# Performance work log

Measured on AMD Instinct MI355X. Metric: run time of the kernel, lower is better.

Reference implementation:

```python
import jax, jax.numpy as jnp
import numpy as np

B, O, GRID = 2048, 48, 112
SIGMA = 5.0


def setup_inputs() -> dict:
    key = jax.random.key(0)
    k1, k2, k3, k4, k5 = jax.random.split(key, 5)
    s = float(GRID - 1)
    xL = jax.random.uniform(k1, (B,), dtype=jnp.float32) * s
    yL = jax.random.uniform(k2, (B,), dtype=jnp.float32) * s
    obj_list = jax.random.uniform(k3, (B, O, 2), dtype=jnp.float32) * s
    obj_num = jax.random.randint(k4, (B,), 0, O + 1, dtype=jnp.int32)
    road_mask = jax.random.randint(k5, (B, GRID, GRID), 0, 2, dtype=jnp.int32)
    return {"xL": xL, "yL": yL, "obj_list": obj_list, "obj_num": obj_num,
            "road_mask": road_mask, "H": GRID, "W": GRID}


def reference(xL, yL, obj_list, obj_num, road_mask, H, W):
    # Faithful vectorization of batch_gaussian_tensor_obj.
    # exp(-(dx^2+dy^2)/(2s^2)) is separable: exp(-dx^2/..) * exp(-dy^2/..),
    # so per-object splats reduce to a batched matmul over the object axis.
    inv = 1.0 / (2.0 * SIGMA * SIGMA)
    x = jnp.arange(H, dtype=jnp.float32)  # row coordinate grid
    y = jnp.arange(W, dtype=jnp.float32)  # col coordinate grid

    # positive goal gaussian, rank-1 outer product per batch element
    gx = jnp.exp(-((x[None, :] - xL[:, None]) ** 2) * inv)  # [B,H]
    gy = jnp.exp(-((y[None, :] - yL[:, None]) ** 2) * inv)  # [B,W]
    goal = gx[:, :, None] * gy[:, None, :]                   # [B,H,W]

    # negative object gaussians; note original swaps xy: xo=xy[1], yo=xy[0]
    xo = obj_list[:, :, 1]  # [B,O] row coords
    yo = obj_list[:, :, 0]  # [B,O] col coords
    ex = jnp.exp(-((x[None, None, :] - xo[:, :, None]) ** 2) * inv)  # [B,O,H]
    ey = jnp.exp(-((y[None, None, :] - yo[:, :, None]) ** 2) * inv)  # [B,O,W]
    valid = (jnp.arange(O)[None, :] < obj_num[:, None]).astype(jnp.float32)  # [B,O]
    obj = jnp.einsum('boh,bow->bhw', ex * valid[:, :, None], ey)     # [B,H,W]

    channel = 0.5 + 0.5 * goal - 0.5 * obj
    channel = jnp.where(road_mask == 0, 0.0, channel)
    return channel
```

## Files before the change

### kernel.cpp

```cpp
#include <hip/hip_runtime.h>

#define GRID_N 112
#define O_MAX 48
#define HW_N (GRID_N * GRID_N)
#define NT 512
#define KPAD 64
#define LSTR 72

typedef _Float16 half8  __attribute__((ext_vector_type(8)));
typedef _Float16 half2v __attribute__((ext_vector_type(2)));
typedef float    f32x4  __attribute__((ext_vector_type(4)));

__global__ __launch_bounds__(NT) void goalmap_kernel(
    const float* __restrict__ xL, const float* __restrict__ yL,
    const float* __restrict__ obj_list, const int* __restrict__ obj_num,
    const int* __restrict__ road_mask, float* __restrict__ out)
{
    constexpr float INV = 1.0f / (2.0f * 5.0f * 5.0f);

    __shared__ float    obj_s[O_MAX * 2];
    __shared__ _Float16 exT[GRID_N * LSTR];
    __shared__ _Float16 eyT[GRID_N * LSTR];

    const int b   = blockIdx.x;
    const int tid = threadIdx.x;
    const int n   = obj_num[b];
    const float xl = xL[b];
    const float yl = yL[b];
    const float* ob = obj_list + (size_t)b * O_MAX * 2;

    if (tid < O_MAX * 2) obj_s[tid] = ob[tid];

    const int lane = tid & 63;
    const int wid  = tid >> 6;
    const int m    = lane & 15;
    const int quad = lane >> 4;

    const int* rm = road_mask + (size_t)b * HW_N;
    float*     op = out       + (size_t)b * HW_N;

    int mpf[7][4];
    if (wid < 7) {
        const int base_h = wid * 16 + quad * 4;
        #pragma unroll
        for (int i = 0; i < 7; ++i) {
            int base = base_h * GRID_N + i * 16 + m;
            #pragma unroll
            for (int r = 0; r < 4; ++r)
                mpf[i][r] = rm[base + r * GRID_N];
        }
    }

    const int ksteps = (n >= 32) ? 2 : 1;
    const int lg     = 3 + ksteps;
    const int kh     = 1 << lg;

    __syncthreads();

    const int nitems = GRID_N << lg;
    for (int i = tid; i < nitems; i += NT) {
        int pos = i >> lg;
        int o0  = (i & (kh - 1)) * 2;
        half2v vx, vy;
        #pragma unroll
        for (int j = 0; j < 2; ++j) {
            int o = o0 + j;
            float valx = 0.f, valy = 0.f;
            if (o <= n) {
                float cx, cy, s;
                if (o < n) { cx = obj_s[o * 2 + 1]; cy = obj_s[o * 2 + 0]; s = -0.5f; }
                else       { cx = xl;               cy = yl;               s =  0.5f; }
                float dx = (float)pos - cx;
                float dy = (float)pos - cy;
                valx = s * __expf(-dx * dx * INV);
                valy =     __expf(-dy * dy * INV);
            }
            vx[j] = (_Float16)valx;
            vy[j] = (_Float16)valy;
        }
        *(half2v*)&exT[pos * LSTR + o0] = vx;
        *(half2v*)&eyT[pos * LSTR + o0] = vy;
    }
    __syncthreads();

    if (wid < 7) {
        const _Float16* arow = &exT[(wid * 16 + m) * LSTR + quad * 8];
        half8 a0 = *(const half8*)arow;
        half8 a1;
        if (ksteps == 2) a1 = *(const half8*)(arow + 32);

        const int h0 = wid * 16 + quad * 4;

        #pragma unroll
        for (int tw = 0; tw < 7; ++tw) {
            const _Float16* brow = &eyT[(tw * 16 + m) * LSTR + quad * 8];
            half8 b0 = *(const half8*)brow;

            f32x4 acc = {0.f, 0.f, 0.f, 0.f};
            acc = __builtin_amdgcn_mfma_f32_16x16x32_f16(a0, b0, acc, 0, 0, 0);
            if (ksteps == 2) {
                half8 b1 = *(const half8*)(brow + 32);
                acc = __builtin_amdgcn_mfma_f32_16x16x32_f16(a1, b1, acc, 0, 0, 0);
            }

            int w0 = tw * 16 + m;
            #pragma unroll
            for (int r = 0; r < 4; ++r) {
                float v = 0.5f + acc[r];
                v = (mpf[tw][r] == 0) ? 0.f : v;
                op[(h0 + r) * GRID_N + w0] = v;
            }
        }
    }
}

extern "C" void kernel_launch(void* const* d_in, const int* in_sizes, int n_in,
                              void* d_out, int out_size, void* d_ws, size_t ws_size,
                              hipStream_t stream) {
    const float* xL        = (const float*)d_in[0];
    const float* yL        = (const float*)d_in[1];
    const float* obj_list  = (const float*)d_in[2];
    const int*   obj_num   = (const int*)d_in[3];
    const int*   road_mask = (const int*)d_in[4];
    float*       out       = (float*)d_out;
    const int B = in_sizes[0];

    goalmap_kernel<<<B, NT, 0, stream>>>(xL, yL, obj_list, obj_num, road_mask, out);
}
```

Measured before the change: 203.2 us.

## Build A operand in registers, shrink block to 7 waves, stream road mask loads

The block shrinks from 8 to 7 waves so every thread takes part in the MFMA stage. Each lane now computes its A-operand (row exp) values directly in registers, which removes the exT shared buffer and the obj_s staging, and the two barriers become a single raw s_barrier. The road-mask prefetch is split: three column tiles load up front and the rest stream inside the MFMA loop, with the aim of lowering register pressure and overlapping loads with compute. The cost is redundant exp evaluations across lanes and hand-placed scheduling barriers.

```diff
diff --git a/kernel.cpp b/kernel.cpp
--- a/kernel.cpp
+++ b/kernel.cpp
@@ -3,8 +3,7 @@
 #define GRID_N 112
 #define O_MAX 48
 #define HW_N (GRID_N * GRID_N)
-#define NT 512
-#define KPAD 64
+#define NT 448
 #define LSTR 72
 
 typedef _Float16 half8  __attribute__((ext_vector_type(8)));
@@ -18,8 +17,6 @@
 {
     constexpr float INV = 1.0f / (2.0f * 5.0f * 5.0f);
 
-    __shared__ float    obj_s[O_MAX * 2];
-    __shared__ _Float16 exT[GRID_N * LSTR];
     __shared__ _Float16 eyT[GRID_N * LSTR];
 
     const int b   = blockIdx.x;
@@ -29,8 +26,6 @@
     const float yl = yL[b];
     const float* ob = obj_list + (size_t)b * O_MAX * 2;
 
-    if (tid < O_MAX * 2) obj_s[tid] = ob[tid];
-
     const int lane = tid & 63;
     const int wid  = tid >> 6;
     const int m    = lane & 15;
@@ -39,77 +34,120 @@
     const int* rm = road_mask + (size_t)b * HW_N;
     float*     op = out       + (size_t)b * HW_N;
 
+    const int ksteps = (n >= 32) ? 2 : 1;
+
+    float eyy0[8], eyy1[8];
+    #pragma unroll
+    for (int it = 0; it < 8; ++it) {
+        int i  = tid + it * NT;
+        int o0 = (i & 31) * 2;
+        eyy0[it] = (o0     < n) ? ob[o0 * 2]     : 0.f;
+        eyy1[it] = (o0 + 1 < n) ? ob[o0 * 2 + 2] : 0.f;
+    }
+    float ax0[8], ax1[8];
+    #pragma unroll
+    for (int j = 0; j < 8; ++j) {
+        int k = quad * 8 + j;
+        ax0[j] = (k < n)      ? ob[k * 2 + 1]        : 0.f;
+        ax1[j] = (k + 32 < n) ? ob[(k + 32) * 2 + 1] : 0.f;
+    }
+
     int mpf[7][4];
-    if (wid < 7) {
-        const int base_h = wid * 16 + quad * 4;
+    const int base_h = wid * 16 + quad * 4;
+    #pragma unroll
+    for (int twp = 0; twp < 3; ++twp) {
+        int base = base_h * GRID_N + twp * 16 + m;
         #pragma unroll
-        for (int i = 0; i < 7; ++i) {
-            int base = base_h * GRID_N + i * 16 + m;
-            #pragma unroll
-            for (int r = 0; r < 4; ++r)
-                mpf[i][r] = rm[base + r * GRID_N];
+        for (int r = 0; r < 4; ++r)
+            mpf[twp][r] = rm[base + r * GRID_N];
+    }
+
+    #pragma unroll
+    for (int it = 0; it < 8; ++it) {
+        int i   = tid + it * NT;
+        int pos = i >> 5;
+        int o0  = (i & 31) * 2;
+        float fp = (float)pos;
+        half2v v;
+        {
+            float val = 0.f;
+            if (o0 <= n) {
+                float cy = (o0 < n) ? eyy0[it] : yl;
+                float d  = fp - cy;
+                val = __expf(-d * d * INV);
+            }
+            v[0] = (_Float16)val;
+        }
+        {
+            int o = o0 + 1;
+            float val = 0.f;
+            if (o <= n) {
+                float cy = (o < n) ? eyy1[it] : yl;
+                float d  = fp - cy;
+                val = __expf(-d * d * INV);
+            }
+            v[1] = (_Float16)val;
+        }
+        *(half2v*)&eyT[pos * LSTR + o0] = v;
+    }
+
+    const float fh = (float)(wid * 16 + m);
+    half8 a0, a1;
+    #pragma unroll
+    for (int j = 0; j < 8; ++j) {
+        int k = quad * 8 + j;
+        float val = 0.f;
+        if (k <= n) {
+            float cx = (k < n) ? ax0[j] : xl;
+            float s  = (k < n) ? -0.5f  : 0.5f;
+            float d  = fh - cx;
+            val = s * __expf(-d * d * INV);
+        }
+        a0[j] = (_Float16)val;
+    }
+    if (ksteps == 2) {
+        #pragma unroll
+        for (int j = 0; j < 8; ++j) {
+            int k = quad * 8 + j + 32;
+            float val = 0.f;
+            if (k <= n) {
+                float cx = (k < n) ? ax1[j] : xl;
+                float s  = (k < n) ? -0.5f  : 0.5f;
+                float d  = fh - cx;
+                val = s * __expf(-d * d * INV);
+            }
+            a1[j] = (_Float16)val;
         }
     }
 
-    const int ksteps = (n >= 32) ? 2 : 1;
-    const int lg     = 3 + ksteps;
-    const int kh     = 1 << lg;
+    __builtin_amdgcn_sched_barrier(0);
+    asm volatile("s_waitcnt lgkmcnt(0)" ::: "memory");
+    __builtin_amdgcn_s_barrier();
+    __builtin_amdgcn_sched_barrier(0);
 
-    __syncthreads();
-
-    const int nitems = GRID_N << lg;
-    for (int i = tid; i < nitems; i += NT) {
-        int pos = i >> lg;
-        int o0  = (i & (kh - 1)) * 2;
-        half2v vx, vy;
+    const int h0 = wid * 16 + quad * 4;
+    #pragma unroll
+    for (int tw = 0; tw < 7; ++tw) {
+        if (tw + 3 < 7) {
+            int base = base_h * GRID_N + (tw + 3) * 16 + m;
+            #pragma unroll
+            for (int r = 0; r < 4; ++r)
+                mpf[tw + 3][r] = rm[base + r * GRID_N];
+        }
+        const _Float16* brow = &eyT[(tw * 16 + m) * LSTR + quad * 8];
+        half8 b0 = *(const half8*)brow;
+        f32x4 acc = {0.f, 0.f, 0.f, 0.f};
+        acc = __builtin_amdgcn_mfma_f32_16x16x32_f16(a0, b0, acc, 0, 0, 0);
+        if (ksteps == 2) {
+            half8 b1 = *(const half8*)(brow + 32);
+            acc = __builtin_amdgcn_mfma_f32_16x16x32_f16(a1, b1, acc, 0, 0, 0);
+        }
+        int w0 = tw * 16 + m;
         #pragma unroll
-        for (int j = 0; j < 2; ++j) {
-            int o = o0 + j;
-            float valx = 0.f, valy = 0.f;
-            if (o <= n) {
-                float cx, cy, s;
-                if (o < n) { cx = obj_s[o * 2 + 1]; cy = obj_s[o * 2 + 0]; s = -0.5f; }
-                else       { cx = xl;               cy = yl;               s =  0.5f; }
-                float dx = (float)pos - cx;
-                float dy = (float)pos - cy;
-                valx = s * __expf(-dx * dx * INV);
-                valy =     __expf(-dy * dy * INV);
-            }
-            vx[j] = (_Float16)valx;
-            vy[j] = (_Float16)valy;
-        }
-        *(half2v*)&exT[pos * LSTR + o0] = vx;
-        *(half2v*)&eyT[pos * LSTR + o0] = vy;
-    }
-    __syncthreads();
-
-    if (wid < 7) {
-        const _Float16* arow = &exT[(wid * 16 + m) * LSTR + quad * 8];
-        half8 a0 = *(const half8*)arow;
-        half8 a1;
-        if (ksteps == 2) a1 = *(const half8*)(arow + 32);
-
-        const int h0 = wid * 16 + quad * 4;
-
-        #pragma unroll
-        for (int tw = 0; tw < 7; ++tw) {
-            const _Float16* brow = &eyT[(tw * 16 + m) * LSTR + quad * 8];
-            half8 b0 = *(const half8*)brow;
-
-            f32x4 acc = {0.f, 0.f, 0.f, 0.f};
-            acc = __builtin_amdgcn_mfma_f32_16x16x32_f16(a0, b0, acc, 0, 0, 0);
-            if (ksteps == 2) {
-                half8 b1 = *(const half8*)(brow + 32);
-                acc = __builtin_amdgcn_mfma_f32_16x16x32_f16(a1, b1, acc, 0, 0, 0);
-            }
-
-            int w0 = tw * 16 + m;
-            #pragma unroll
-            for (int r = 0; r < 4; ++r) {
-                float v = 0.5f + acc[r];
-                v = (mpf[tw][r] == 0) ? 0.f : v;
-                op[(h0 + r) * GRID_N + w0] = v;
-            }
+        for (int r = 0; r < 4; ++r) {
+            float v = 0.5f + acc[r];
+            v = (mpf[tw][r] == 0) ? 0.f : v;
+            op[(h0 + r) * GRID_N + w0] = v;
         }
     }
 }
```

After: 210.2 us. 3.4% more time.
